# Performance work log

Hardware: AMD Instinct MI355X
Metric: run time of the kernel (lower is better)

Reference implementation:

```python
import jax, jax.numpy as jnp
import numpy as np

EMB_DIM = 1024
NUM_HEADS = 16
HEAD_DIM = EMB_DIM // NUM_HEADS


def setup_inputs() -> dict:
    key = jax.random.key(0)
    ks = jax.random.split(key, 9)
    B, S = 2, 2048
    s = 1.0 / np.sqrt(EMB_DIM)
    return {
        "x": jax.random.normal(ks[0], (B, S, EMB_DIM), jnp.float32),
        "Wq": jax.random.normal(ks[1], (EMB_DIM, EMB_DIM), jnp.float32) * s,
        "bq": jnp.zeros((EMB_DIM,), jnp.float32),
        "Wk": jax.random.normal(ks[2], (EMB_DIM, EMB_DIM), jnp.float32) * s,
        "bk": jnp.zeros((EMB_DIM,), jnp.float32),
        "Wv": jax.random.normal(ks[3], (EMB_DIM, EMB_DIM), jnp.float32) * s,
        "bv": jnp.zeros((EMB_DIM,), jnp.float32),
        "Wo": jax.random.normal(ks[4], (EMB_DIM, EMB_DIM), jnp.float32) * s,
        "bo": jnp.zeros((EMB_DIM,), jnp.float32),
    }


def reference(x, Wq, bq, Wk, bk, Wv, bv, Wo, bo):
    B, S, E = x.shape
    H, D = NUM_HEADS, HEAD_DIM
    # QKV projections (torch Linear: x @ W.T + b; here W is stored as [in,out])
    q = (x @ Wq + bq).reshape(B, S, H, D).transpose(0, 2, 1, 3)  # [B,H,S,D]
    k = (x @ Wk + bk).reshape(B, S, H, D).transpose(0, 2, 1, 3)
    v = (x @ Wv + bv).reshape(B, S, H, D).transpose(0, 2, 1, 3)
    # raw scores, then causal mask with -inf, then scale inside softmax
    scores = jnp.einsum("bhqd,bhkd->bhqk", q, k)  # [B,H,S,S]
    causal = jnp.tril(jnp.ones((S, S), bool))
    scores = jnp.where(causal, scores, -jnp.inf)
    attn = jax.nn.softmax(scores / np.sqrt(D), axis=-1)
    # dropout prob is 0.0 (eval-equivalent), so it's identity
    ctx = jnp.einsum("bhqk,bhkd->bhqd", attn, v)  # [B,H,S,D]
    ctx = ctx.transpose(0, 2, 1, 3).reshape(B, S, E)
    return ctx @ Wo + bo
```

## Files before the change

kernel.cpp:

```cpp
#include <hip/hip_runtime.h>
#include <hip/hip_bf16.h>
#include <cstdint>

#define NB   2
#define NS   2048
#define NE   1024
#define NH   16
#define ND   64
#define BS   (NB*NS)

typedef float f32x4 __attribute__((ext_vector_type(4)));
typedef __bf16 bf16x8 __attribute__((ext_vector_type(8)));

#define MFMA16(a,b,c) __builtin_amdgcn_mfma_f32_16x16x32_bf16((a),(b),(c),0,0,0)

#define KCF 0.18033688011112042f

typedef const __attribute__((address_space(1))) unsigned int* gas_u32;
typedef __attribute__((address_space(3))) unsigned int* las_u32;

__device__ __forceinline__ void gload_lds16(const void* g, void* l) {
    __builtin_amdgcn_global_load_lds((gas_u32)g, (las_u32)l, 16, 0, 0);
}

__device__ __forceinline__ unsigned short bf16_bits(float f) {
    __bf16 h = (__bf16)f;
    return __builtin_bit_cast(unsigned short, h);
}
__device__ __forceinline__ float bits_bf16(unsigned short u) {
    return (float)__builtin_bit_cast(__bf16, u);
}

__global__ __launch_bounds__(256) void prep_kernel(const float* __restrict__ x,
                                                   __bf16* __restrict__ xb,
                                                   const float* __restrict__ W0,
                                                   const float* __restrict__ W1,
                                                   const float* __restrict__ W2,
                                                   const float* __restrict__ W3,
                                                   __bf16* __restrict__ wt) {
    __shared__ float tile[32][33];
    int z = blockIdx.z;
    int tx = threadIdx.x, ty = threadIdx.y;
    if (z == 0) {
        size_t base = ((size_t)(blockIdx.y * 32 + blockIdx.x) * 256 +
                       ty * 32 + tx) * 16;
        const float4* p = (const float4*)(x + base);
        float4 a = p[0], b = p[1], c = p[2], d = p[3];
        bf16x8 v0, v1;
        v0[0]=(__bf16)a.x; v0[1]=(__bf16)a.y; v0[2]=(__bf16)a.z; v0[3]=(__bf16)a.w;
        v0[4]=(__bf16)b.x; v0[5]=(__bf16)b.y; v0[6]=(__bf16)b.z; v0[7]=(__bf16)b.w;
        v1[0]=(__bf16)c.x; v1[1]=(__bf16)c.y; v1[2]=(__bf16)c.z; v1[3]=(__bf16)c.w;
        v1[4]=(__bf16)d.x; v1[5]=(__bf16)d.y; v1[6]=(__bf16)d.z; v1[7]=(__bf16)d.w;
        *(bf16x8*)(xb + base) = v0;
        *(bf16x8*)(xb + base + 8) = v1;
        return;
    }
    int w = z - 1;
    const float* W = (w==0) ? W0 : (w==1) ? W1 : (w==2) ? W2 : W3;
    __bf16* out = wt + (size_t)w * NE * NE;
    int k0 = blockIdx.y * 32, n0 = blockIdx.x * 32;
    #pragma unroll
    for (int i = 0; i < 4; i++)
        tile[ty + 8*i][tx] = W[(size_t)(k0 + ty + 8*i) * NE + n0 + tx];
    __syncthreads();
    #pragma unroll
    for (int i = 0; i < 4; i++)
        out[(size_t)(n0 + ty + 8*i) * NE + k0 + tx] = (__bf16)tile[tx][ty + 8*i];
}

template<int EPI>
__global__ __launch_bounds__(256, 2) void gemm128_kernel(
        const __bf16* __restrict__ A, const __bf16* __restrict__ Bt,
        const float* __restrict__ bias0, const float* __restrict__ bias1,
        const float* __restrict__ bias2,
        __bf16* __restrict__ o0, __bf16* __restrict__ o1, __bf16* __restrict__ o2,
        float* __restrict__ fout) {
    __shared__ __align__(16) char smem[2][16384];
    const int K = 1024;
    int t = threadIdx.x;
    int wave = t >> 6, lane = t & 63;
    int wm = wave >> 1, wn = wave & 1;
    int lg = lane >> 4, li = lane & 15;
    int m0 = blockIdx.y * 128, n0 = blockIdx.x * 128;

    const __bf16* Ag = A + (size_t)(m0 + (t >> 2)) * K + (t & 3) * 8;
    const __bf16* Bg = Bt + (size_t)(n0 + (t >> 2)) * K + (t & 3) * 8;

#define GSTAGE(K0, BI) do {                                             \
        gload_lds16(Ag + (K0),          smem[BI] +         t * 16);     \
        gload_lds16(Ag + 64 * K + (K0), smem[BI] +  4096 + t * 16);     \
        gload_lds16(Bg + (K0),          smem[BI] +  8192 + t * 16);     \
        gload_lds16(Bg + 64 * K + (K0), smem[BI] + 12288 + t * 16);     \
    } while (0)

    GSTAGE(0, 0);
    f32x4 acc[4][4] = {};
    __syncthreads();

    for (int k0 = 0; k0 < K; k0 += 32) {
        int cur = (k0 >> 5) & 1;
        if (k0 + 32 < K) GSTAGE(k0 + 32, cur ^ 1);

        const __bf16* As = (const __bf16*)smem[cur];
        const __bf16* Bs = (const __bf16*)(smem[cur] + 8192);
        bf16x8 af[4], bfr[4];
        #pragma unroll
        for (int i = 0; i < 4; i++)
            af[i] = *(const bf16x8*)(As + (size_t)(wm*64 + i*16 + li) * 32 + lg * 8);
        #pragma unroll
        for (int i = 0; i < 4; i++)
            bfr[i] = *(const bf16x8*)(Bs + (size_t)(wn*64 + i*16 + li) * 32 + lg * 8);
        #pragma unroll
        for (int i = 0; i < 4; i++)
            #pragma unroll
            for (int j = 0; j < 4; j++)
                acc[i][j] = MFMA16(af[i], bfr[j], acc[i][j]);

        __syncthreads();
    }
#undef GSTAGE

    #pragma unroll
    for (int i = 0; i < 4; i++) {
        int mrow = m0 + wm * 64 + i * 16 + lg * 4;
        #pragma unroll
        for (int j = 0; j < 4; j++) {
            int n = n0 + wn * 64 + j * 16 + li;
            if (EPI == 0) {
                int widx = n >> 10, nn = n & 1023;
                const float* bb = (widx == 0) ? bias0 : (widx == 1) ? bias1 : bias2;
                float bv = bb[nn];
                int h = nn >> 6, d = nn & 63;
                int bidx = mrow >> 11, s0 = mrow & 2047;
                if (widx == 2) {
                    ushort4 pk;
                    pk.x = bf16_bits(acc[i][j][0] + bv);
                    pk.y = bf16_bits(acc[i][j][1] + bv);
                    pk.z = bf16_bits(acc[i][j][2] + bv);
                    pk.w = bf16_bits(acc[i][j][3] + bv);
                    *(ushort4*)(o2 + (((size_t)bidx * NH + h) * ND + d) * NS + s0) = pk;
                } else {
                    __bf16* dst = (widx == 0) ? o0 : o1;
                    float scl = (widx == 0) ? KCF : 1.0f;
                    #pragma unroll
                    for (int r = 0; r < 4; r++)
                        dst[(((size_t)bidx * NH + h) * NS + s0 + r) * ND + d] =
                            (__bf16)((acc[i][j][r] + bv) * scl);
                }
            } else {
                float bv = bias0[n];
                #pragma unroll
                for (int r = 0; r < 4; r++)
                    fout[(size_t)(mrow + r) * NE + n] = acc[i][j][r] + bv;
            }
        }
    }
}

__global__ __launch_bounds__(256) void attn_kernel(const __bf16* __restrict__ qb,
                                                   const __bf16* __restrict__ kb,
                                                   const __bf16* __restrict__ vt,
                                                   __bf16* __restrict__ ctx,
                                                   __bf16* __restrict__ Opart,
                                                   float* __restrict__ lbuf,
                                                   int split) {
    __shared__ __align__(16) char kbuf[2][8192];
    __shared__ __align__(16) char vbuf[2][8192];
    __shared__ __align__(16) ushort pbuf[4][1024];

    int t = threadIdx.x;
    int wave = t >> 6, lane = t & 63;
    int lg = lane >> 4, li = lane & 15;
    int bh = blockIdx.y, b = bh >> 4, h = bh & 15;
    int bx = blockIdx.x;

    int qt, c, nch;
    if (!split) {
        qt = bx; c = 0; nch = 1;
    } else {
        int a = (bx < 8) ? 0 : (bx < 24) ? 1 : (bx < 48) ? 2 : 3;
        int seg = (a == 0) ? 0 : (a == 1) ? 8 : (a == 2) ? 24 : 48;
        int idx = bx - seg;
        int dv = a + 1;
        qt = a * 8 + idx / dv;
        c  = idx % dv;
        nch = a + 1;
    }
    int jlo = c * 8;
    int jhi = min(jlo + 8, qt + 1);
    int nt = jhi - jlo;
    bool direct = (nch == 1);

    int qw = qt * 64 + wave * 16;
    const __bf16* Q  = qb + ((size_t)bh * NS + qw) * ND;
    const __bf16* Kg = kb + (size_t)bh * NS * ND;
    const __bf16* Vg = vt + (size_t)bh * ND * NS;

    int sr = t >> 3;
    int sg = (t & 7) ^ (sr & 7);
    const __bf16* Ks0 = Kg + (size_t)sr * ND + sg * 8;
    const __bf16* Ks1 = Kg + (size_t)(32 + sr) * ND + sg * 8;
    const __bf16* Vs0 = Vg + (size_t)sr * NS + sg * 8;
    const __bf16* Vs1 = Vg + (size_t)(32 + sr) * NS + sg * 8;

#define STAGE_KV(J, BI) do {                                              \
        gload_lds16(Ks0 + (size_t)(J) * 4096, &kbuf[BI][t * 16]);         \
        gload_lds16(Ks1 + (size_t)(J) * 4096, &kbuf[BI][4096 + t * 16]);  \
        gload_lds16(Vs0 + (size_t)(J) * 64,   &vbuf[BI][t * 16]);         \
        gload_lds16(Vs1 + (size_t)(J) * 64,   &vbuf[BI][4096 + t * 16]);  \
    } while (0)

    bf16x8 aq0 = *(const bf16x8*)(Q + li * ND + lg * 8);
    bf16x8 aq1 = *(const bf16x8*)(Q + li * ND + 32 + lg * 8);

    STAGE_KV(jlo, 0);

    f32x4 o[4] = {};
    float lpart = 0.f;
    int swz = (li & 7) << 4;
    int qg = qw + li;

    char* pw = (char*)&pbuf[wave][0];
    char* pwr = pw + li * 128 + (lg & 1) * 8;
    int k6base = (lg >> 1);

    __syncthreads();

    for (int it = 0; it < nt; ++it) {
        int j = jlo + it;
        int cur = it & 1;
        if (it + 1 < nt) STAGE_KV(j + 1, cur ^ 1);

        const char* kt = (const char*)kbuf[cur];
        f32x4 sc[4];
        #pragma unroll
        for (int h4 = 0; h4 < 4; ++h4) {
            const char* kr = kt + (h4 * 16 + li) * 128;
            bf16x8 b0 = *(const bf16x8*)(kr + ((lg << 4) ^ swz));
            bf16x8 b1 = *(const bf16x8*)(kr + (((4 + lg) << 4) ^ swz));
            f32x4 z = {};
            z = MFMA16(b0, aq0, z);
            z = MFMA16(b1, aq1, z);
            sc[h4] = z;
        }

        if (j == qt) {
            #pragma unroll
            for (int h4 = 0; h4 < 4; ++h4)
                #pragma unroll
                for (int r = 0; r < 4; ++r) {
                    int kv = j * 64 + h4 * 16 + lg * 4 + r;
                    if (kv > qg) sc[h4][r] = -1e30f;
                }
        }

        #pragma unroll
        for (int h4 = 0; h4 < 4; ++h4) {
            #pragma unroll
            for (int r = 0; r < 4; ++r) {
                float p = exp2f(sc[h4][r]);
                sc[h4][r] = p;
                lpart += p;
            }
        }

        #pragma unroll
        for (int h4 = 0; h4 < 4; ++h4) {
            uint2 w64;
            w64.x = (unsigned int)bf16_bits(sc[h4][0]) |
                    ((unsigned int)bf16_bits(sc[h4][1]) << 16);
            w64.y = (unsigned int)bf16_bits(sc[h4][2]) |
                    ((unsigned int)bf16_bits(sc[h4][3]) << 16);
            int k6 = h4 * 2 + k6base;
            *(uint2*)(pwr + (((k6 ^ (li & 7)) << 4))) = w64;
        }
        asm volatile("s_waitcnt lgkmcnt(0)" ::: "memory");

        const char* vtl = (const char*)vbuf[cur];
        #pragma unroll
        for (int ks = 0; ks < 2; ++ks) {
            int ch = (ks * 4 + lg) << 4;
            bf16x8 pf = *(const bf16x8*)(pw + li * 128 + (ch ^ swz));
            #pragma unroll
            for (int i = 0; i < 4; ++i) {
                bf16x8 vf = *(const bf16x8*)(vtl + (i * 16 + li) * 128 + (ch ^ swz));
                o[i] = MFMA16(vf, pf, o[i]);
            }
        }
        __syncthreads();
    }
#undef STAGE_KV

    float lsum = lpart + __shfl_xor(lpart, 16);
    lsum += __shfl_xor(lsum, 32);

    if (direct) {
        float inv = 1.f / lsum;
        __bf16* dst = ctx + ((size_t)b * NS + qg) * NE + h * ND;
        #pragma unroll
        for (int i = 0; i < 4; ++i) {
            ushort4 pack;
            pack.x = bf16_bits(o[i][0] * inv);
            pack.y = bf16_bits(o[i][1] * inv);
            pack.z = bf16_bits(o[i][2] * inv);
            pack.w = bf16_bits(o[i][3] * inv);
            *(ushort4*)(dst + i * 16 + lg * 4) = pack;
        }
    } else {
        int slot = bh * 80 + bx;
        int ql = wave * 16 + li;
        __bf16* Op = Opart + (size_t)slot * 4096 + ql * 64;
        #pragma unroll
        for (int i = 0; i < 4; ++i) {
            ushort4 pack;
            pack.x = bf16_bits(o[i][0]);
            pack.y = bf16_bits(o[i][1]);
            pack.z = bf16_bits(o[i][2]);
            pack.w = bf16_bits(o[i][3]);
            *(ushort4*)(Op + i * 16 + lg * 4) = pack;
        }
        if (lg == 0)
            lbuf[(size_t)slot * 64 + ql] = lsum;
    }
}

__global__ __launch_bounds__(256) void combine_kernel(const __bf16* __restrict__ Opart,
                                                      const float* __restrict__ lbuf,
                                                      __bf16* __restrict__ ctx) {
    int qt = 8 + blockIdx.x;
    int bh = blockIdx.y, b = bh >> 4, h = bh & 15;
    int a = qt >> 3, bq = qt & 7;
    int off = (a + 1) * (4 * a + bq);
    int nch = a + 1;
    int slotbase = bh * 80 + off;
    int t = threadIdx.x;
    int q = t >> 2, dg = t & 3;

    float L = 0.f;
    #pragma unroll
    for (int c = 0; c < 4; ++c)
        if (c < nch)
            L += lbuf[(size_t)(slotbase + c) * 64 + q];
    float invL = 1.f / L;

    float acc[16] = {};
    #pragma unroll
    for (int c = 0; c < 4; ++c)
        if (c < nch) {
            const uint4* src = (const uint4*)(Opart + (size_t)(slotbase + c) * 4096 +
                                              q * 64 + dg * 16);
            #pragma unroll
            for (int half = 0; half < 2; ++half) {
                uint4 v = src[half];
                unsigned int w[4] = {v.x, v.y, v.z, v.w};
                #pragma unroll
                for (int u = 0; u < 4; ++u) {
                    acc[half * 8 + u * 2]     += bits_bf16((ushort)(w[u] & 0xffff));
                    acc[half * 8 + u * 2 + 1] += bits_bf16((ushort)(w[u] >> 16));
                }
            }
        }

    int qg = qt * 64 + q;
    __bf16* dst = ctx + ((size_t)b * NS + qg) * NE + h * ND + dg * 16;
    #pragma unroll
    for (int half = 0; half < 2; ++half) {
        ushort4 pack;
        pack.x = bf16_bits(acc[half * 8 + 0] * invL);
        pack.y = bf16_bits(acc[half * 8 + 1] * invL);
        pack.z = bf16_bits(acc[half * 8 + 2] * invL);
        pack.w = bf16_bits(acc[half * 8 + 3] * invL);
        ushort4 pack2;
        pack2.x = bf16_bits(acc[half * 8 + 4] * invL);
        pack2.y = bf16_bits(acc[half * 8 + 5] * invL);
        pack2.z = bf16_bits(acc[half * 8 + 6] * invL);
        pack2.w = bf16_bits(acc[half * 8 + 7] * invL);
        *(ushort4*)(dst + half * 8) = pack;
        *(ushort4*)(dst + half * 8 + 4) = pack2;
    }
}

extern "C" void kernel_launch(void* const* d_in, const int* in_sizes, int n_in,
                              void* d_out, int out_size, void* d_ws, size_t ws_size,
                              hipStream_t stream) {
    (void)in_sizes; (void)n_in; (void)out_size;
    const float* x  = (const float*)d_in[0];
    const float* Wq = (const float*)d_in[1];
    const float* bq = (const float*)d_in[2];
    const float* Wk = (const float*)d_in[3];
    const float* bk = (const float*)d_in[4];
    const float* Wv = (const float*)d_in[5];
    const float* bv = (const float*)d_in[6];
    const float* Wo = (const float*)d_in[7];
    const float* bo = (const float*)d_in[8];
    float* out = (float*)d_out;

    char* ws = (char*)d_ws;
    const size_t MB = 1024 * 1024;
    __bf16* xb  = (__bf16*)(ws);
    __bf16* wt  = (__bf16*)(ws +  8 * MB);
    __bf16* qb  = (__bf16*)(ws + 16 * MB);
    __bf16* kb  = (__bf16*)(ws + 24 * MB);
    __bf16* vtb = (__bf16*)(ws + 32 * MB);
    __bf16* ctx = xb;
    __bf16* Opart = (__bf16*)(ws + 40 * MB);
    float*  lbuf  = (float*)(ws + 40 * MB + 20971520);
    const size_t NEED = 40 * MB + 20971520 + 655360;

    int split = (ws_size >= NEED) ? 1 : 0;

    prep_kernel<<<dim3(32, 32, 5), dim3(32, 8), 0, stream>>>(
        x, xb, Wq, Wk, Wv, Wo, wt);
    gemm128_kernel<0><<<dim3(24, 32), 256, 0, stream>>>(
        xb, wt, bq, bk, bv, qb, kb, vtb, nullptr);
    attn_kernel<<<dim3(split ? 80 : 32, NB * NH), 256, 0, stream>>>(
        qb, kb, vtb, ctx, Opart, lbuf, split);
    if (split)
        combine_kernel<<<dim3(24, NB * NH), 256, 0, stream>>>(Opart, lbuf, ctx);
    gemm128_kernel<1><<<dim3(8, 32), 256, 0, stream>>>(
        ctx, wt + 3 * (size_t)NE * NE, bo, nullptr, nullptr, nullptr, nullptr,
        nullptr, out);
}
```

Baseline: 193.6 us.

## Refine barriers, swizzle GEMM block order, reverse attention tile order, add setprio

```diff
diff --git a/kernel.cpp b/kernel.cpp
--- a/kernel.cpp
+++ b/kernel.cpp
@@ -81,7 +81,11 @@
     int wave = t >> 6, lane = t & 63;
     int wm = wave >> 1, wn = wave & 1;
     int lg = lane >> 4, li = lane & 15;
-    int m0 = blockIdx.y * 128, n0 = blockIdx.x * 128;
+
+    int bid = blockIdx.y * gridDim.x + blockIdx.x;
+    int cpx = (gridDim.x * gridDim.y) >> 3;
+    int swzb = (bid & 7) * cpx + (bid >> 3);
+    int m0 = (swzb / gridDim.x) * 128, n0 = (swzb % gridDim.x) * 128;
 
     const __bf16* Ag = A + (size_t)(m0 + (t >> 2)) * K + (t & 3) * 8;
     const __bf16* Bg = Bt + (size_t)(n0 + (t >> 2)) * K + (t & 3) * 8;
@@ -99,7 +103,13 @@
 
     for (int k0 = 0; k0 < K; k0 += 32) {
         int cur = (k0 >> 5) & 1;
-        if (k0 + 32 < K) GSTAGE(k0 + 32, cur ^ 1);
+        if (k0 + 32 < K) {
+            GSTAGE(k0 + 32, cur ^ 1);
+            asm volatile("s_waitcnt vmcnt(4)" ::: "memory");
+        } else {
+            asm volatile("s_waitcnt vmcnt(0)" ::: "memory");
+        }
+        __builtin_amdgcn_s_barrier();
 
         const __bf16* As = (const __bf16*)smem[cur];
         const __bf16* Bs = (const __bf16*)(smem[cur] + 8192);
@@ -116,7 +126,9 @@
             for (int j = 0; j < 4; j++)
                 acc[i][j] = MFMA16(af[i], bfr[j], acc[i][j]);
 
-        __syncthreads();
+        asm volatile("s_waitcnt lgkmcnt(0)" ::: "memory");
+        __builtin_amdgcn_sched_barrier(0);
+        __builtin_amdgcn_s_barrier();
     }
 #undef GSTAGE
 
@@ -172,7 +184,7 @@
     int wave = t >> 6, lane = t & 63;
     int lg = lane >> 4, li = lane & 15;
     int bh = blockIdx.y, b = bh >> 4, h = bh & 15;
-    int bx = blockIdx.x;
+    int bx = (split ? 79 : 31) - blockIdx.x;
 
     int qt, c, nch;
     if (!split) {
@@ -229,10 +241,17 @@
     for (int it = 0; it < nt; ++it) {
         int j = jlo + it;
         int cur = it & 1;
-        if (it + 1 < nt) STAGE_KV(j + 1, cur ^ 1);
+        if (it + 1 < nt) {
+            STAGE_KV(j + 1, cur ^ 1);
+            asm volatile("s_waitcnt vmcnt(4)" ::: "memory");
+        } else {
+            asm volatile("s_waitcnt vmcnt(0)" ::: "memory");
+        }
+        __builtin_amdgcn_s_barrier();
 
         const char* kt = (const char*)kbuf[cur];
         f32x4 sc[4];
+        __builtin_amdgcn_s_setprio(1);
         #pragma unroll
         for (int h4 = 0; h4 < 4; ++h4) {
             const char* kr = kt + (h4 * 16 + li) * 128;
@@ -243,6 +262,7 @@
             z = MFMA16(b1, aq1, z);
             sc[h4] = z;
         }
+        __builtin_amdgcn_s_setprio(0);
 
         if (j == qt) {
             #pragma unroll
@@ -275,8 +295,10 @@
             *(uint2*)(pwr + (((k6 ^ (li & 7)) << 4))) = w64;
         }
         asm volatile("s_waitcnt lgkmcnt(0)" ::: "memory");
+        __builtin_amdgcn_sched_barrier(0);
 
         const char* vtl = (const char*)vbuf[cur];
+        __builtin_amdgcn_s_setprio(1);
         #pragma unroll
         for (int ks = 0; ks < 2; ++ks) {
             int ch = (ks * 4 + lg) << 4;
@@ -287,7 +309,11 @@
                 o[i] = MFMA16(vf, pf, o[i]);
             }
         }
-        __syncthreads();
+        __builtin_amdgcn_s_setprio(0);
+
+        asm volatile("s_waitcnt lgkmcnt(0)" ::: "memory");
+        __builtin_amdgcn_sched_barrier(0);
+        __builtin_amdgcn_s_barrier();
     }
 #undef STAGE_KV
 
```

Result: no change. 194.8 us (+0.6%).
